# Performance work log

Hardware: AMD Instinct MI355X
Metric: run time of the kernel (lower is better)

Reference implementation:

```python
import jax, jax.numpy as jnp
import numpy as np

FP8_MAX = 448.0  # max representable magnitude in float8_e4m3fn
EPS = 1e-12


def setup_inputs() -> dict:
    key = jax.random.key(0)
    k1, k2, k3 = jax.random.split(key, 3)
    B, S, DIN, DOUT = 8, 4096, 1024, 1024
    x = jax.random.normal(k1, (B, S, DIN), dtype=jnp.float32)
    weight = jax.random.normal(k2, (DOUT, DIN), dtype=jnp.float32) * (1.0 / np.sqrt(DIN))
    bias = jax.random.normal(k3, (DOUT,), dtype=jnp.float32) * 0.01
    return {"x": x, "weight": weight, "bias": bias}


def _quantize_fp8(t):
    # per-tensor dynamic scale: amax / 448, clamped
    scale = jnp.maximum(jnp.max(jnp.abs(t)) / FP8_MAX, EPS).astype(jnp.float32)
    t_fp8 = (t / scale).astype(jnp.float8_e4m3fn)
    return t_fp8, scale


def reference(x, weight, bias):
    in_features = weight.shape[1]
    out_features = weight.shape[0]
    # quantize weights (mirrors quantize_weights())
    w_fp8, w_scale = _quantize_fp8(weight)
    # dynamic activation quantization
    x_flat = x.reshape(-1, in_features)  # [M, K]
    x_fp8, x_scale = _quantize_fp8(x_flat)
    # scaled fp8 GEMM: accumulate in fp32, apply per-tensor scales (torch._scaled_mm)
    out = jnp.einsum(
        "mk,nk->mn",
        x_fp8.astype(jnp.float32),
        w_fp8.astype(jnp.float32),
    ) * (x_scale * w_scale)
    out = out.reshape(*x.shape[:-1], out_features)
    return out + bias
```

## Files before the change

### kernel.cpp

```cpp
#include <hip/hip_runtime.h>
#include <cstdint>
#include <cstddef>

typedef float f32x4 __attribute__((ext_vector_type(4)));
typedef long  lx2   __attribute__((ext_vector_type(2)));

#define PXB 1024
#define PWB 64
#define QWB 64

__device__ __forceinline__ void async_copy16(const uint8_t* g, uint8_t* s) {
    __builtin_amdgcn_global_load_lds(
        (const __attribute__((address_space(1))) void*)g,
        (__attribute__((address_space(3))) void*)s,
        16 , 0 , 0 );
}

__device__ __forceinline__ float block_max(float m, float* scr) {
#pragma unroll
    for (int o = 32; o > 0; o >>= 1) m = fmaxf(m, __shfl_down(m, o, 64));
    const int lane = threadIdx.x & 63, wid = threadIdx.x >> 6;
    if (lane == 0) scr[wid] = m;
    __syncthreads();
    const int nw = blockDim.x >> 6;
    m = scr[0];
    for (int j = 1; j < nw; ++j) m = fmaxf(m, scr[j]);
    return m;
}

__global__ void amax_partials(const float4* __restrict__ x, int nx4,
                              const float4* __restrict__ w, int nw4,
                              float* __restrict__ part) {
    __shared__ float scr[8];
    const int b = blockIdx.x;
    const float4* p;
    int n4, nb, bi;
    if (b < PXB) { p = x; n4 = nx4; nb = PXB; bi = b; }
    else         { p = w; n4 = nw4; nb = PWB; bi = b - PXB; }
    float m = 0.0f;
    for (int i = bi * blockDim.x + threadIdx.x; i < n4; i += nb * blockDim.x) {
        float4 v = p[i];
        m = fmaxf(m, fmaxf(fmaxf(fabsf(v.x), fabsf(v.y)),
                           fmaxf(fabsf(v.z), fabsf(v.w))));
    }
    m = block_max(m, scr);
    if (threadIdx.x == 0) part[b] = m;
}

__global__ void quant_w_kernel(const float4* __restrict__ w, int nw16,
                               const float* __restrict__ part,
                               int4* __restrict__ wq) {
    __shared__ float scr[8];
    float m = 0.0f;
    for (int i = threadIdx.x; i < PWB; i += blockDim.x)
        m = fmaxf(m, part[PXB + i]);
    m = block_max(m, scr);
    const float r = 1.0f / fmaxf(m / 448.0f, 1e-12f);

    for (int i = blockIdx.x * blockDim.x + threadIdx.x; i < nw16;
         i += QWB * blockDim.x) {
        int4 o;
#pragma unroll
        for (int j = 0; j < 4; ++j) {
            float4 v = w[i * 4 + j];
            int p = 0;
            p = __builtin_amdgcn_cvt_pk_fp8_f32(v.x * r, v.y * r, p, false);
            p = __builtin_amdgcn_cvt_pk_fp8_f32(v.z * r, v.w * r, p, true);
            ((int*)&o)[j] = p;
        }
        wq[i] = o;
    }
}

__global__ __launch_bounds__(256) void gemm_fp8_kernel(
    const float* __restrict__ A32,
    const uint8_t* __restrict__ B,
    const float* __restrict__ bias,
    const float* __restrict__ part,
    float* __restrict__ out,
    int M, int N, int K) {
    __shared__ long lds64[2048];
    uint8_t* Abase = (uint8_t*)lds64;
    uint8_t* Bbase = Abase + 8192;

    const int tid  = threadIdx.x;
    const int l    = tid & 63;
    const int w    = tid >> 6;
    const int lm   = l & 15;
    const int quad = l >> 4;
    const int wm   = (w >> 1) * 64;
    const int wn   = (w & 1) * 64;

    int bx = blockIdx.x, by = blockIdx.y;
    if (gridDim.x == 8) {
        const int lin = blockIdx.x + (blockIdx.y << 3);
        const int c = lin & 7;
        const int k = lin >> 3;
        bx = k & 7;
        by = (k & ~7) | c;
    }
    const size_t am0 = (size_t)by * 128;
    const size_t bn0 = (size_t)bx * 128;

    const int arow = tid >> 4;
    const int acol = (tid & 15) * 4;
    const float* aptr = A32 + (am0 + arow) * (size_t)K + acol;

    f32x4 av[8];
#pragma unroll
    for (int j = 0; j < 8; ++j)
        av[j] = *(const f32x4*)(aptr + (size_t)j * 16 * K);

    float* scr = (float*)lds64;
    float mx = 0.0f, mw = 0.0f;
    for (int i = tid; i < PXB; i += 256) mx = fmaxf(mx, part[i]);
    for (int i = tid; i < PWB; i += 256) mw = fmaxf(mw, part[PXB + i]);
    mx = block_max(mx, scr);
    mw = block_max(mw, scr + 8);
    const float sx = fmaxf(mx / 448.0f, 1e-12f);
    const float sw = fmaxf(mw / 448.0f, 1e-12f);
    const float scale = sx * sw;
    const float rq = 1.0f / sx;
    __syncthreads();

    f32x4 acc[4][4];
#pragma unroll
    for (int i = 0; i < 4; ++i)
#pragma unroll
        for (int j = 0; j < 4; ++j) acc[i][j] = (f32x4)0.0f;

    const int slot0 = w * 64 + l;

    for (int kt = 0; kt < K; kt += 64) {
#pragma unroll
        for (int i = 0; i < 2; ++i) {
            const int s    = i * 256 + slot0;
            const int row  = s >> 2;
            const int chnk = s & 3;
            async_copy16(B + (bn0 + row) * K + kt + chnk * 16,
                         Bbase + (i * 4 + w) * 1024);
        }
#pragma unroll
        for (int j = 0; j < 8; ++j) {
            int p = 0;
            p = __builtin_amdgcn_cvt_pk_fp8_f32(av[j].x * rq, av[j].y * rq, p, false);
            p = __builtin_amdgcn_cvt_pk_fp8_f32(av[j].z * rq, av[j].w * rq, p, true);
            *(int*)(Abase + (j * 16 + arow) * 64 + acol) = p;
        }
        __syncthreads();

        lx2 a[4], b[4];
#pragma unroll
        for (int t = 0; t < 4; ++t) {
            a[t] = *(const lx2*)&lds64[(wm + t * 16 + lm) * 8 + quad * 2];
            b[t] = *(const lx2*)&lds64[1024 + (wn + t * 16 + lm) * 8 + quad * 2];
        }
        if (kt + 64 < K) {
            const float* ap = aptr + (kt + 64);
#pragma unroll
            for (int j = 0; j < 8; ++j)
                av[j] = *(const f32x4*)(ap + (size_t)j * 16 * K);
        }
#pragma unroll
        for (int ks = 0; ks < 2; ++ks)
#pragma unroll
            for (int mt = 0; mt < 4; ++mt)
#pragma unroll
                for (int nt = 0; nt < 4; ++nt)
                    acc[mt][nt] = __builtin_amdgcn_mfma_f32_16x16x32_fp8_fp8(
                        a[mt][ks], b[nt][ks], acc[mt][nt], 0, 0, 0);
        __syncthreads();
    }

#pragma unroll
    for (int nt = 0; nt < 4; ++nt) {
        const int n = (int)bn0 + wn + nt * 16 + lm;
        const float bv = bias[n];
#pragma unroll
        for (int mt = 0; mt < 4; ++mt) {
            const size_t mrow = am0 + wm + mt * 16 + quad * 4;
#pragma unroll
            for (int r = 0; r < 4; ++r) {
                out[(mrow + r) * (size_t)N + n] = acc[mt][nt][r] * scale + bv;
            }
        }
    }
}

extern "C" void kernel_launch(void* const* d_in, const int* in_sizes, int n_in,
                              void* d_out, int out_size, void* d_ws,
                              size_t ws_size, hipStream_t stream) {
    const float* x      = (const float*)d_in[0];
    const float* weight = (const float*)d_in[1];
    const float* bias   = (const float*)d_in[2];
    float* out          = (float*)d_out;

    const int nx = in_sizes[0];
    const int nw = in_sizes[1];
    const int N  = in_sizes[2];
    const int K  = nw / N;
    const int M  = nx / K;

    float* part     = (float*)d_ws;
    uint8_t* w_fp8  = (uint8_t*)d_ws + 8192;

    amax_partials<<<PXB + PWB, 256, 0, stream>>>(
        (const float4*)x, nx / 4, (const float4*)weight, nw / 4, part);
    quant_w_kernel<<<QWB, 256, 0, stream>>>(
        (const float4*)weight, nw / 16, part, (int4*)w_fp8);
    gemm_fp8_kernel<<<dim3(N / 128, M / 128), 256, 0, stream>>>(
        x, w_fp8, bias, part, out, M, N, K);
}
```

Measured before the change: 297.3 us.

## Double-buffer LDS tiles in FP8 GEMM with one barrier per K-step

Doubles the LDS A/B buffers so the next K-tile's weight async copies and activation FP8 conversion are written into the alternate buffer while MFMAs run on the current one. The two __syncthreads per iteration become a single barrier with a partial vmcnt wait that leaves the prefetched activation loads outstanding. MFMA sections are bracketed with s_setprio to favour the compute wave. This uses twice the LDS and more register pressure from the extra in-flight loads, which can lower occupancy.

```diff
diff --git a/kernel.cpp b/kernel.cpp
--- a/kernel.cpp
+++ b/kernel.cpp
@@ -15,6 +15,14 @@
         (__attribute__((address_space(3))) void*)s,
         16 , 0 , 0 );
 }
+
+#define BARRIER_VM(N)                                                     \
+    do {                                                                  \
+        asm volatile("s_waitcnt vmcnt(" #N ") lgkmcnt(0)" ::: "memory");  \
+        __builtin_amdgcn_sched_barrier(0);                                \
+        __builtin_amdgcn_s_barrier();                                     \
+        __builtin_amdgcn_sched_barrier(0);                                \
+    } while (0)
 
 __device__ __forceinline__ float block_max(float m, float* scr) {
 #pragma unroll
@@ -79,9 +87,7 @@
     const float* __restrict__ part,
     float* __restrict__ out,
     int M, int N, int K) {
-    __shared__ long lds64[2048];
-    uint8_t* Abase = (uint8_t*)lds64;
-    uint8_t* Bbase = Abase + 8192;
+    __shared__ long lds64[4112];
 
     const int tid  = threadIdx.x;
     const int l    = tid & 63;
@@ -94,10 +100,10 @@
     int bx = blockIdx.x, by = blockIdx.y;
     if (gridDim.x == 8) {
         const int lin = blockIdx.x + (blockIdx.y << 3);
-        const int c = lin & 7;
-        const int k = lin >> 3;
-        bx = k & 7;
-        by = (k & ~7) | c;
+        const int c0 = lin & 7;
+        const int k0 = lin >> 3;
+        bx = k0 & 7;
+        by = (k0 & ~7) | c0;
     }
     const size_t am0 = (size_t)by * 128;
     const size_t bn0 = (size_t)bx * 128;
@@ -111,7 +117,7 @@
     for (int j = 0; j < 8; ++j)
         av[j] = *(const f32x4*)(aptr + (size_t)j * 16 * K);
 
-    float* scr = (float*)lds64;
+    float* scr = (float*)&lds64[4096];
     float mx = 0.0f, mw = 0.0f;
     for (int i = tid; i < PXB; i += 256) mx = fmaxf(mx, part[i]);
     for (int i = tid; i < PWB; i += 256) mw = fmaxf(mw, part[PXB + i]);
@@ -121,7 +127,6 @@
     const float sw = fmaxf(mw / 448.0f, 1e-12f);
     const float scale = sx * sw;
     const float rq = 1.0f / sx;
-    __syncthreads();
 
     f32x4 acc[4][4];
 #pragma unroll
@@ -131,36 +136,64 @@
 
     const int slot0 = w * 64 + l;
 
-    for (int kt = 0; kt < K; kt += 64) {
+    {
+        uint8_t* A0 = (uint8_t*)lds64;
+        uint8_t* B0 = (uint8_t*)(lds64 + 1024);
 #pragma unroll
         for (int i = 0; i < 2; ++i) {
-            const int s    = i * 256 + slot0;
-            const int row  = s >> 2;
-            const int chnk = s & 3;
-            async_copy16(B + (bn0 + row) * K + kt + chnk * 16,
-                         Bbase + (i * 4 + w) * 1024);
+            const int s = i * 256 + slot0;
+            async_copy16(B + (bn0 + (s >> 2)) * (size_t)K + (s & 3) * 16,
+                         B0 + (i * 4 + w) * 1024);
         }
 #pragma unroll
         for (int j = 0; j < 8; ++j) {
             int p = 0;
             p = __builtin_amdgcn_cvt_pk_fp8_f32(av[j].x * rq, av[j].y * rq, p, false);
             p = __builtin_amdgcn_cvt_pk_fp8_f32(av[j].z * rq, av[j].w * rq, p, true);
-            *(int*)(Abase + (j * 16 + arow) * 64 + acol) = p;
-        }
-        __syncthreads();
+            *(int*)(A0 + (j * 16 + arow) * 64 + acol) = p;
+        }
+#pragma unroll
+        for (int j = 0; j < 8; ++j)
+            av[j] = *(const f32x4*)(aptr + 64 + (size_t)j * 16 * K);
+        BARRIER_VM(8);
+    }
+
+    int c = 0;
+    for (int kt = 0; kt < K; kt += 64) {
+        long* Ab = lds64 + (c ? 2048 : 0);
+        long* Bb = Ab + 1024;
+        const bool haveNext = (kt + 64 < K);
+
+        if (haveNext) {
+            uint8_t* An = (uint8_t*)(lds64 + (c ? 0 : 2048));
+            uint8_t* Bn = An + 8192;
+#pragma unroll
+            for (int i = 0; i < 2; ++i) {
+                const int s = i * 256 + slot0;
+                async_copy16(B + (bn0 + (s >> 2)) * (size_t)K + (kt + 64) + (s & 3) * 16,
+                             Bn + (i * 4 + w) * 1024);
+            }
+#pragma unroll
+            for (int j = 0; j < 8; ++j) {
+                int p = 0;
+                p = __builtin_amdgcn_cvt_pk_fp8_f32(av[j].x * rq, av[j].y * rq, p, false);
+                p = __builtin_amdgcn_cvt_pk_fp8_f32(av[j].z * rq, av[j].w * rq, p, true);
+                *(int*)(An + (j * 16 + arow) * 64 + acol) = p;
+            }
+            if (kt + 128 < K) {
+#pragma unroll
+                for (int j = 0; j < 8; ++j)
+                    av[j] = *(const f32x4*)(aptr + (kt + 128) + (size_t)j * 16 * K);
+            }
+        }
 
         lx2 a[4], b[4];
 #pragma unroll
         for (int t = 0; t < 4; ++t) {
-            a[t] = *(const lx2*)&lds64[(wm + t * 16 + lm) * 8 + quad * 2];
-            b[t] = *(const lx2*)&lds64[1024 + (wn + t * 16 + lm) * 8 + quad * 2];
-        }
-        if (kt + 64 < K) {
-            const float* ap = aptr + (kt + 64);
-#pragma unroll
-            for (int j = 0; j < 8; ++j)
-                av[j] = *(const f32x4*)(ap + (size_t)j * 16 * K);
-        }
+            a[t] = *(const lx2*)&Ab[(wm + t * 16 + lm) * 8 + quad * 2];
+            b[t] = *(const lx2*)&Bb[(wn + t * 16 + lm) * 8 + quad * 2];
+        }
+        __builtin_amdgcn_s_setprio(1);
 #pragma unroll
         for (int ks = 0; ks < 2; ++ks)
 #pragma unroll
@@ -169,7 +202,13 @@
                 for (int nt = 0; nt < 4; ++nt)
                     acc[mt][nt] = __builtin_amdgcn_mfma_f32_16x16x32_fp8_fp8(
                         a[mt][ks], b[nt][ks], acc[mt][nt], 0, 0, 0);
-        __syncthreads();
+        __builtin_amdgcn_s_setprio(0);
+
+        if (haveNext) {
+            if (kt + 128 < K) { BARRIER_VM(8); }
+            else             { BARRIER_VM(0); }
+        }
+        c ^= 1;
     }
 
 #pragma unroll
```

After: 323.6 us. 1.09x slower.
